# Kernel tuning notes

Measured on AMD Instinct MI355X. Metric: run time of the kernel, lower is better.

The kernel has to match this reference:

```python
import jax, jax.numpy as jnp
import numpy as np

B, C_IN, T_IN = 128, 128, 2500
C_OUT, K, STRIDE, PAD = 64, 27, 4, 13  # T_out = 625
BN_EPS = 1e-5
SURROGATE_ALPHA = 4.0


def binarize_weight(w):
    """1-bit (XNOR-Net style) weight quantization with straight-through estimator.
    w: (O, I, K). Per-output-channel scale = mean |w|."""
    alpha = jnp.mean(jnp.abs(w), axis=(1, 2), keepdims=True)
    wq = jnp.sign(w) * alpha
    return w + jax.lax.stop_gradient(wq - w)


def spike(x):
    """Heaviside spike with sigmoid surrogate gradient (STE)."""
    hard = (x > 0).astype(x.dtype)
    soft = jax.nn.sigmoid(SURROGATE_ALPHA * x)
    return soft + jax.lax.stop_gradient(hard - soft)


def setup_inputs() -> dict:
    key = jax.random.key(0)
    ks = jax.random.split(key, 8)
    scale_conv = 1.0 / np.sqrt(C_IN * K)
    scale_lin = 1.0 / np.sqrt(C_OUT)
    return {
        "x": jax.random.normal(ks[0], (B, C_IN, T_IN), dtype=jnp.float32),
        "conv_w": jax.random.normal(ks[1], (C_OUT, C_IN, K), dtype=jnp.float32) * scale_conv,
        "conv_b": jnp.zeros((C_OUT,), dtype=jnp.float32),
        "bn_gamma": jnp.ones((C_OUT,), dtype=jnp.float32),
        "bn_beta": jnp.zeros((C_OUT,), dtype=jnp.float32),
        "bn_mean": jax.random.normal(ks[2], (C_OUT,), dtype=jnp.float32) * 0.1,
        "bn_var": jax.random.uniform(ks[3], (C_OUT,), dtype=jnp.float32, minval=0.5, maxval=1.5),
        "wq": jax.random.normal(ks[4], (C_OUT, C_OUT), dtype=jnp.float32) * scale_lin,
        "wk": jax.random.normal(ks[5], (C_OUT, C_OUT), dtype=jnp.float32) * scale_lin,
        "wv": jax.random.normal(ks[6], (C_OUT, C_OUT), dtype=jnp.float32) * scale_lin,
        "wo": jax.random.normal(ks[7], (C_OUT, C_OUT), dtype=jnp.float32) * scale_lin,
    }


def reference(x, conv_w, conv_b, bn_gamma, bn_beta, bn_mean, bn_var, wq, wk, wv, wo):
    # --- 1-bit quantized conv1d, stride 4 ---
    w_bin = binarize_weight(conv_w)
    y = jax.lax.conv_general_dilated(
        x, w_bin, window_strides=(STRIDE,), padding=[(PAD, PAD)],
        dimension_numbers=("NCH", "OIH", "NCH"))
    y = y + conv_b[None, :, None]  # (B, C_OUT, 625)

    # --- BatchNorm1d (inference stats) + ELU ---
    inv = jax.lax.rsqrt(bn_var + BN_EPS)
    y = (y - bn_mean[None, :, None]) * (inv * bn_gamma)[None, :, None] + bn_beta[None, :, None]
    y = jax.nn.elu(y)

    # --- Global spiking attention (single head) ---
    s = spike(y)                                   # (B, C, T) binary spikes
    q = jnp.einsum("oc,bct->bot", wq, s)           # (B, C, T)
    k = jnp.einsum("oc,bct->bot", wk, s)
    v = jnp.einsum("oc,bct->bot", wv, y)
    scores = jnp.einsum("bct,bcs->bts", q, k) / jnp.sqrt(jnp.asarray(C_OUT, y.dtype))
    attn = jax.nn.softmax(scores, axis=-1)         # (B, T, T)
    ctx = jnp.einsum("bts,bcs->bct", attn, v)      # (B, C, T)
    out = y + jnp.einsum("oc,bct->bot", wo, ctx)   # residual
    return out
```

## Files before the change

kernel.cpp:

```cpp
#include <hip/hip_runtime.h>
#include <math.h>

#define B_    128
#define CIN   128
#define TIN   2500
#define COUT  64
#define KW    27
#define TOUT  625
#define TPAD  640
#define CTT   32
#define GROWS 152

typedef __bf16 bf16x8 __attribute__((ext_vector_type(8)));
typedef float  f32x4  __attribute__((ext_vector_type(4)));
typedef float  f32x16 __attribute__((ext_vector_type(16)));

__device__ __forceinline__ unsigned short f32_to_bf16_rne(float v) {
    unsigned u = __float_as_uint(v);
    u += 0x7FFFu + ((u >> 16) & 1u);
    return (unsigned short)(u >> 16);
}

__device__ __forceinline__ f32x4 mfma_bf16(bf16x8 a, bf16x8 b, f32x4 c) {
    return __builtin_amdgcn_mfma_f32_16x16x32_bf16(a, b, c, 0, 0, 0);
}

__global__ void prep_kernel(const float* __restrict__ w,
                            const float* __restrict__ wq, const float* __restrict__ wk,
                            const float* __restrict__ wv, const float* __restrict__ wo,
                            const float* __restrict__ conv_b, const float* __restrict__ gamma_,
                            const float* __restrict__ beta_, const float* __restrict__ mean_,
                            const float* __restrict__ var_,
                            unsigned* __restrict__ sgn2,
                            unsigned short* __restrict__ w3_h, unsigned short* __restrict__ w3_l,
                            unsigned short* __restrict__ wo_h, unsigned short* __restrict__ wo_l,
                            float* __restrict__ scA, float* __restrict__ scB) {
    int blk = blockIdx.x, tid = threadIdx.x;
    if (blk < 64) {
        __shared__ float red[256];
        const float* wrow = w + (size_t)blk * (CIN * KW);
        float s = 0.f;
        for (int idx = tid; idx < CIN * KW; idx += 256) s += fabsf(wrow[idx]);
        red[tid] = s;
        __syncthreads();
        for (int st = 128; st > 0; st >>= 1) {
            if (tid < st) red[tid] += red[tid + st];
            __syncthreads();
        }
        if (tid == 0) {
            float alpha = red[0] / (float)(CIN * KW);
            float inv = rsqrtf(var_[blk] + 1e-5f);
            float G = gamma_[blk] * inv;
            scA[blk] = alpha * G;
            scB[blk] = (conv_b[blk] - mean_[blk]) * G + beta_[blk];
        }
        for (int t = tid; t < KW * 4; t += 256) {
            int kk = t >> 2, kg = t & 3;
            unsigned u = 0;
#pragma unroll
            for (int cs = 0; cs < 4; cs++) {
#pragma unroll
                for (int j = 0; j < 8; j++) {
                    int c = cs * 32 + kg * 8 + j;
                    float v = wrow[c * KW + kk];
                    unsigned bit = (v > 0.f) ? 0u : 1u;
                    u |= bit << (cs * 8 + j);
                }
            }
            sgn2[(kk * 4 + kg) * 64 + blk] = u;
        }
    } else if (blk < 67) {
        const float* srcs[3] = {wq, wk, wv};
        const float* src = srcs[blk - 64];
        unsigned short* dh = w3_h + (size_t)(blk - 64) * 4096;
        unsigned short* dl = w3_l + (size_t)(blk - 64) * 4096;
        for (int idx = tid; idx < 4096; idx += 256) {
            float v = src[idx];
            unsigned short h = f32_to_bf16_rne(v);
            float hf = __uint_as_float((unsigned)h << 16);
            dh[idx] = h;
            dl[idx] = f32_to_bf16_rne(v - hf);
        }
    } else {
        for (int idx = tid; idx < 4096; idx += 256) {
            float v = wo[idx];
            unsigned short h = f32_to_bf16_rne(v);
            float hf = __uint_as_float((unsigned)h << 16);
            wo_h[idx] = h;
            wo_l[idx] = f32_to_bf16_rne(v - hf);
        }
    }
}

__global__ __launch_bounds__(256, 4) void conv_kernel(
    const float* __restrict__ x, const unsigned* __restrict__ sgn2,
    const float* __restrict__ scA, const float* __restrict__ scB,
    const unsigned short* __restrict__ w3_h, const unsigned short* __restrict__ w3_l,
    float* __restrict__ y_out,
    unsigned short* __restrict__ q_h, unsigned short* __restrict__ k_h,
    unsigned short* __restrict__ vT_h)
{
    __shared__ __align__(16) unsigned short xhi[GROWS * 128];
    __shared__ __align__(16) unsigned long long sgnlut[16];
    unsigned short* y_sh = xhi;
    unsigned short* s_sh = xhi + 2048;
    unsigned short* q_sh = xhi + 4096;
    unsigned short* k_sh = xhi + 6144;
    unsigned short* v_sh = xhi + 8192;
    float* part_sh = (float*)(xhi + 10240);

    int tid = threadIdx.x;
    int id = blockIdx.x + 20 * blockIdx.y;
    int nid = (id & 7) * 320 + (id >> 3);
    int b = nid / 20;
    int t0 = (nid - b * 20) * CTT;

    if (tid < 16) {
        unsigned long long e = 0;
#pragma unroll
        for (int j = 0; j < 4; ++j) {
            unsigned long long h = ((tid >> j) & 1) ? 0xBF80ull : 0x3F80ull;
            e |= h << (16 * j);
        }
        sgnlut[tid] = e;
    }

    const float* xb = x + (size_t)b * CIN * TIN;
    int gbase = 4 * t0 - 13;
    for (int task = tid; task < 16 * GROWS; task += 256) {
        int c8 = task / GROWS, gl = task - c8 * GROWS;
        int g = gbase + gl;
        bool valid = (gl < 151) && ((unsigned)g < (unsigned)TIN);
        float vs[8];
#pragma unroll
        for (int j = 0; j < 8; j++)
            vs[j] = valid ? xb[(size_t)(c8 * 8 + j) * TIN + g] : 0.f;
        union { unsigned u[4]; uint4 q; } H;
#pragma unroll
        for (int j = 0; j < 4; j++) {
            unsigned short h0 = f32_to_bf16_rne(vs[2 * j]);
            unsigned short h1 = f32_to_bf16_rne(vs[2 * j + 1]);
            H.u[j] = (unsigned)h0 | ((unsigned)h1 << 16);
        }
        int c8p = c8 ^ ((gl >> 2) & 15);
        *(uint4*)(xhi + gl * 128 + c8p * 8) = H.q;
    }
    __syncthreads();

    int wave = tid >> 6, lane = tid & 63;
    int oh = wave & 1, ch = wave >> 1;
    int o0w = oh * 32;
    int lo = lane & 31;
    int kg1 = lane >> 5;

    f32x16 acc = {0.f};
    const unsigned* sgb = sgn2 + o0w + lo;
    unsigned w0 = sgb[kg1 * 64];
    unsigned w1 = sgb[(kg1 + 2) * 64];

#pragma unroll 1
    for (int kk = 0; kk < KW; ++kk) {
        unsigned n0 = 0, n1 = 0;
        if (kk < KW - 1) {
            n0 = sgb[((kk + 1) * 4 + kg1) * 64];
            n1 = sgb[((kk + 1) * 4 + kg1 + 2) * 64];
        }
        int gl = 4 * lo + kk;
        int rot = (gl >> 2) & 15;
        const unsigned short* xr = xhi + gl * 128;
#pragma unroll
        for (int ks = 0; ks < 4; ++ks) {
            int oct = ch * 8 + ks * 2 + kg1;
            int c8p = oct ^ rot;
            bf16x8 bx = *(const bf16x8*)(xr + c8p * 8);
            unsigned wsel = (ks & 1) ? w1 : w0;
            unsigned byte = (wsel >> (8 * (ch * 2 + (ks >> 1)))) & 0xFFu;
            union { unsigned long long u[2]; bf16x8 v; } A;
            A.u[0] = sgnlut[byte & 15u];
            A.u[1] = sgnlut[byte >> 4];
            acc = __builtin_amdgcn_mfma_f32_32x32x16_bf16(A.v, bx, acc, 0, 0, 0);
        }
        w0 = n0; w1 = n1;
    }
    __syncthreads();

    if (ch == 1) {
        float* p = part_sh + oh * 1024 + lane;
#pragma unroll
        for (int r = 0; r < 16; ++r) p[r * 64] = acc[r];
    }
    __syncthreads();

    if (ch == 0) {
        const float* p = part_sh + oh * 1024 + lane;
        int t_g = t0 + lo;
        bool tv = t_g < TOUT;
#pragma unroll
        for (int g2 = 0; g2 < 4; ++g2) {
            unsigned long long yp = 0, sp = 0;
#pragma unroll
            for (int j = 0; j < 4; ++j) {
                int r = g2 * 4 + j;
                float v = acc[r] + p[r * 64];
                int o = o0w + 4 * kg1 + 8 * g2 + j;
                float s = v * scA[o] + scB[o];
                float yv = s > 0.f ? s : expm1f(s);
                if (tv) {
                    y_out[((size_t)b * COUT + o) * TOUT + t_g] = yv;
                    yp |= (unsigned long long)f32_to_bf16_rne(yv) << (16 * j);
                    if (yv > 0.f) sp |= 0x3F80ull << (16 * j);
                }
            }
            int c8 = 4 * oh + g2;
            int idx = lo * 64 + ((c8 ^ (lo & 7)) << 3) + 4 * kg1;
            *(unsigned long long*)(y_sh + idx) = yp;
            *(unsigned long long*)(s_sh + idx) = sp;
        }
    }
    __syncthreads();

    int quad = lane >> 4, col = lane & 15;
    int o0 = wave * 16;
    bf16x8 sf[2][2], yf[2][2];
#pragma unroll
    for (int tt = 0; tt < 2; ++tt)
#pragma unroll
        for (int ks = 0; ks < 2; ++ks) {
            int tl = tt * 16 + col;
            int idx = tl * 64 + (((ks * 4 + quad) ^ (tl & 7)) << 3);
            sf[tt][ks] = *(const bf16x8*)(s_sh + idx);
            yf[tt][ks] = *(const bf16x8*)(y_sh + idx);
        }
    size_t wofs = (size_t)(o0 + col) * 64 + quad * 8;
    f32x4 qa[2], ka[2], va[2];
#pragma unroll
    for (int tt = 0; tt < 2; ++tt) {
        qa[tt] = (f32x4){0.f, 0.f, 0.f, 0.f};
        ka[tt] = (f32x4){0.f, 0.f, 0.f, 0.f};
        va[tt] = (f32x4){0.f, 0.f, 0.f, 0.f};
    }
#pragma unroll
    for (int ks = 0; ks < 2; ++ks) {
        bf16x8 aqh = *(const bf16x8*)(w3_h + wofs + ks * 32);
        bf16x8 aql = *(const bf16x8*)(w3_l + wofs + ks * 32);
        bf16x8 akh = *(const bf16x8*)(w3_h + 4096 + wofs + ks * 32);
        bf16x8 akl = *(const bf16x8*)(w3_l + 4096 + wofs + ks * 32);
        bf16x8 avh = *(const bf16x8*)(w3_h + 8192 + wofs + ks * 32);
        bf16x8 avl = *(const bf16x8*)(w3_l + 8192 + wofs + ks * 32);
#pragma unroll
        for (int tt = 0; tt < 2; ++tt) {
            qa[tt] = mfma_bf16(aqh, sf[tt][ks], qa[tt]);
            qa[tt] = mfma_bf16(aql, sf[tt][ks], qa[tt]);
            ka[tt] = mfma_bf16(akh, sf[tt][ks], ka[tt]);
            ka[tt] = mfma_bf16(akl, sf[tt][ks], ka[tt]);
            va[tt] = mfma_bf16(avh, yf[tt][ks], va[tt]);
            va[tt] = mfma_bf16(avl, yf[tt][ks], va[tt]);
        }
    }
    int c8w = (o0 >> 3) + (quad >> 1);
    int cof = (quad & 1) * 4;
#pragma unroll
    for (int tt = 0; tt < 2; ++tt) {
        int tl = tt * 16 + col;
        int idx = tl * 64 + ((c8w ^ (tl & 7)) << 3) + cof;
        unsigned long long qp = 0, kp = 0;
#pragma unroll
        for (int r = 0; r < 4; ++r) {
            qp |= (unsigned long long)f32_to_bf16_rne(qa[tt][r]) << (16 * r);
            kp |= (unsigned long long)f32_to_bf16_rne(ka[tt][r]) << (16 * r);
        }
        *(unsigned long long*)(q_sh + idx) = qp;
        *(unsigned long long*)(k_sh + idx) = kp;
#pragma unroll
        for (int r = 0; r < 4; ++r) {
            int c = o0 + quad * 4 + r;
            int vidx = c * 32 + (((tt * 2 + (col >> 3)) ^ quad) << 3) + (col & 7);
            v_sh[vidx] = f32_to_bf16_rne(va[tt][r]);
        }
    }
    __syncthreads();

    {
        int tl = tid >> 3, seg = tid & 7;
        int idx = tl * 64 + ((seg ^ (tl & 7)) << 3);
        uint4 qv = *(const uint4*)(q_sh + idx);
        uint4 kv = *(const uint4*)(k_sh + idx);
        size_t go = ((size_t)b * TPAD + t0 + tl) * 64 + seg * 8;
        *(uint4*)(q_h + go) = qv;
        *(uint4*)(k_h + go) = kv;
        int c = tid >> 2, ts = tid & 3;
        int vidx = c * 32 + ((ts ^ ((c >> 2) & 3)) << 3);
        uint4 vv = *(const uint4*)(v_sh + vidx);
        *(uint4*)(vT_h + ((size_t)b * 64 + c) * TPAD + t0 + ts * 8) = vv;
    }
}

__global__ __launch_bounds__(512, 3) void attn_kernel(
    const unsigned short* __restrict__ q_h, const unsigned short* __restrict__ k_h,
    const unsigned short* __restrict__ vT_h, const float* __restrict__ y,
    const unsigned short* __restrict__ wo_h, const unsigned short* __restrict__ wo_l,
    float* __restrict__ out)
{
    __shared__ __align__(16) float sc_sh[16 * 648];
    __shared__ float ctx_sh[2 * 64 * 17];
    __shared__ float rden[16];

    int tid = threadIdx.x;
    int id = blockIdx.x + 40 * blockIdx.y;
    int nid = (id & 7) * 640 + (id >> 3);
    int b = nid / 40;
    int t0 = (nid - b * 40) * 16;

    int wave = tid >> 6, lane = tid & 63;
    int quad = lane >> 4, nlo = lane & 15;

    const unsigned short* qb = q_h + ((size_t)b * TPAD + t0 + nlo) * 64 + quad * 8;
    bf16x8 qa0 = *(const bf16x8*)(qb);
    bf16x8 qa1 = *(const bf16x8*)(qb + 32);
    const unsigned short* kbase = k_h + (size_t)b * TPAD * 64 + quad * 8;
#pragma unroll 5
    for (int nt = 0; nt < 5; ++nt) {
        int s = wave * 80 + nt * 16 + nlo;
        const unsigned short* krow = kbase + (size_t)s * 64;
        bf16x8 kb0 = *(const bf16x8*)(krow);
        bf16x8 kb1 = *(const bf16x8*)(krow + 32);
        f32x4 acc = {0.f, 0.f, 0.f, 0.f};
        acc = mfma_bf16(qa0, kb0, acc);
        acc = mfma_bf16(qa1, kb1, acc);
#pragma unroll
        for (int r = 0; r < 4; ++r)
            sc_sh[(quad * 4 + r) * 648 + s] = acc[r] * 0.125f;
    }
    __syncthreads();

    int ti1 = tid >> 5, sg = tid & 31;
    float* srow = &sc_sh[ti1 * 648];
    float mx = -3.0e38f;
    for (int s = sg; s < TOUT; s += 32) mx = fmaxf(mx, srow[s]);
#pragma unroll
    for (int off = 16; off >= 1; off >>= 1) mx = fmaxf(mx, __shfl_xor(mx, off));

    unsigned short* prow = (unsigned short*)srow;
    float sum = 0.f;
#pragma unroll
    for (int k2 = 0; k2 < 10; ++k2) {
        int s = 2 * sg + 64 * k2;
        float2 v2 = *(const float2*)(srow + s);
        float e0 = (s     < TOUT) ? __expf(v2.x - mx) : 0.f;
        float e1 = (s + 1 < TOUT) ? __expf(v2.y - mx) : 0.f;
        sum += e0 + e1;
        unsigned u0 = __float_as_uint(e0); u0 += 0x7FFFu + ((u0 >> 16) & 1u);
        unsigned u1 = __float_as_uint(e1); u1 += 0x7FFFu + ((u1 >> 16) & 1u);
        *(unsigned*)(prow + s) = (u0 >> 16) | (u1 & 0xFFFF0000u);
    }
#pragma unroll
    for (int off = 16; off >= 1; off >>= 1) sum += __shfl_xor(sum, off);
    if (sg == 0) rden[ti1] = 1.f / sum;
    __syncthreads();

    int cw = (wave & 3) * 16, kh = wave >> 2;
    const unsigned short* vb = vT_h + ((size_t)b * 64 + cw + nlo) * TPAD;
    const unsigned short* pb = (const unsigned short*)sc_sh + nlo * 1296;
    f32x4 cacc = {0.f, 0.f, 0.f, 0.f};
    int ks0 = kh * 10;
#pragma unroll 5
    for (int i = 0; i < 10; ++i) {
        int ks = ks0 + i;
        bf16x8 pv = *(const bf16x8*)(pb + ks * 32 + quad * 8);
        bf16x8 v8 = *(const bf16x8*)(vb + ks * 32 + quad * 8);
        cacc = mfma_bf16(pv, v8, cacc);
    }
#pragma unroll
    for (int r = 0; r < 4; ++r)
        ctx_sh[kh * 1088 + (cw + nlo) * 17 + quad * 4 + r] = cacc[r] * rden[quad * 4 + r];
    __syncthreads();

    if (wave < 4) {
        const unsigned short* woh = wo_h + (size_t)(wave * 16 + nlo) * 64 + quad * 8;
        const unsigned short* wol = wo_l + (size_t)(wave * 16 + nlo) * 64 + quad * 8;
        f32x4 oacc = {0.f, 0.f, 0.f, 0.f};
#pragma unroll
        for (int ks = 0; ks < 2; ++ks) {
            union { unsigned short u[8]; bf16x8 v; } Bc;
#pragma unroll
            for (int j = 0; j < 8; ++j) {
                int c = ks * 32 + quad * 8 + j;
                float cv = ctx_sh[c * 17 + nlo] + ctx_sh[1088 + c * 17 + nlo];
                Bc.u[j] = f32_to_bf16_rne(cv);
            }
            bf16x8 ah = *(const bf16x8*)(woh + ks * 32);
            bf16x8 al = *(const bf16x8*)(wol + ks * 32);
            oacc = mfma_bf16(ah, Bc.v, oacc);
            oacc = mfma_bf16(al, Bc.v, oacc);
        }
        int t_g = t0 + nlo;
        if (t_g < TOUT) {
#pragma unroll
            for (int r = 0; r < 4; ++r) {
                int o = wave * 16 + quad * 4 + r;
                size_t off = ((size_t)b * COUT + o) * TOUT + t_g;
                out[off] = y[off] + oacc[r];
            }
        }
    }
}

extern "C" void kernel_launch(void* const* d_in, const int* in_sizes, int n_in,
                              void* d_out, int out_size, void* d_ws, size_t ws_size,
                              hipStream_t stream) {
    const float* x        = (const float*)d_in[0];
    const float* conv_w   = (const float*)d_in[1];
    const float* conv_b   = (const float*)d_in[2];
    const float* bn_gamma = (const float*)d_in[3];
    const float* bn_beta  = (const float*)d_in[4];
    const float* bn_mean  = (const float*)d_in[5];
    const float* bn_var   = (const float*)d_in[6];
    const float* wq       = (const float*)d_in[7];
    const float* wk       = (const float*)d_in[8];
    const float* wv       = (const float*)d_in[9];
    const float* wo       = (const float*)d_in[10];
    float* out = (float*)d_out;
    float* ws  = (float*)d_ws;

    unsigned* sgn2        = (unsigned*)ws;
    float* scA            = ws + 110656;
    float* scB            = ws + 110720;
    unsigned short* w3_h  = (unsigned short*)(ws + 110848);
    unsigned short* w3_l  = (unsigned short*)(ws + 116992);
    unsigned short* wo_h  = (unsigned short*)(ws + 123136);
    unsigned short* wo_l  = (unsigned short*)(ws + 125184);
    float* yb             = ws + 131072;
    unsigned short* q_h   = (unsigned short*)(ws + 5251072);
    unsigned short* k_h   = (unsigned short*)(ws + 7872512);
    unsigned short* vT_h  = (unsigned short*)(ws + 10493952);

    hipLaunchKernelGGL(prep_kernel, dim3(68), dim3(256), 0, stream,
                       conv_w, wq, wk, wv, wo, conv_b, bn_gamma, bn_beta, bn_mean, bn_var,
                       sgn2, w3_h, w3_l, wo_h, wo_l, scA, scB);
    hipLaunchKernelGGL(conv_kernel, dim3(20, 128), dim3(256), 0, stream,
                       x, sgn2, scA, scB, w3_h, w3_l, yb, q_h, k_h, vT_h);
    hipLaunchKernelGGL(attn_kernel, dim3(40, 128), dim3(512), 0, stream,
                       q_h, k_h, vT_h, yb, wo_h, wo_l, out);
}
```

Baseline: 427.0 us.

## Compute softmax in registers from MFMA accumulators with bf16 LDS probabilities

Scaling, row max, exponentials and row sums are now done directly on the QK^T MFMA accumulators in registers. Per-wave partial maxima and sums are combined through small LDS arrays instead of a full fp32 score buffer. Only bf16 probabilities are written to LDS, roughly halving the score buffer and dropping one full pass over it. The launch-bounds occupancy hint rises from 3 to 8 blocks, which forces a tighter register budget and risks spills.

```diff
diff --git a/kernel.cpp b/kernel.cpp
--- a/kernel.cpp
+++ b/kernel.cpp
@@ -295,15 +295,16 @@
     }
 }
 
-__global__ __launch_bounds__(512, 3) void attn_kernel(
+__global__ __launch_bounds__(512, 8) void attn_kernel(
     const unsigned short* __restrict__ q_h, const unsigned short* __restrict__ k_h,
     const unsigned short* __restrict__ vT_h, const float* __restrict__ y,
     const unsigned short* __restrict__ wo_h, const unsigned short* __restrict__ wo_l,
     float* __restrict__ out)
 {
-    __shared__ __align__(16) float sc_sh[16 * 648];
+    __shared__ __align__(16) unsigned short P_lds[16 * 648];
+    __shared__ __align__(16) float pmax_sh[16 * 8];
+    __shared__ __align__(16) float psum_sh[16 * 8];
     __shared__ float ctx_sh[2 * 64 * 17];
-    __shared__ float rden[16];
 
     int tid = threadIdx.x;
     int id = blockIdx.x + 40 * blockIdx.y;
@@ -318,49 +319,91 @@
     bf16x8 qa0 = *(const bf16x8*)(qb);
     bf16x8 qa1 = *(const bf16x8*)(qb + 32);
     const unsigned short* kbase = k_h + (size_t)b * TPAD * 64 + quad * 8;
+    f32x4 acc[5];
 #pragma unroll 5
     for (int nt = 0; nt < 5; ++nt) {
         int s = wave * 80 + nt * 16 + nlo;
         const unsigned short* krow = kbase + (size_t)s * 64;
         bf16x8 kb0 = *(const bf16x8*)(krow);
         bf16x8 kb1 = *(const bf16x8*)(krow + 32);
-        f32x4 acc = {0.f, 0.f, 0.f, 0.f};
-        acc = mfma_bf16(qa0, kb0, acc);
-        acc = mfma_bf16(qa1, kb1, acc);
+        f32x4 a = {0.f, 0.f, 0.f, 0.f};
+        a = mfma_bf16(qa0, kb0, a);
+        a = mfma_bf16(qa1, kb1, a);
+        acc[nt] = a;
+    }
+
+    float rmx[4] = {-3.0e38f, -3.0e38f, -3.0e38f, -3.0e38f};
+#pragma unroll
+    for (int nt = 0; nt < 5; ++nt) {
+        int s = wave * 80 + nt * 16 + nlo;
+        bool v = s < TOUT;
+#pragma unroll
+        for (int r = 0; r < 4; ++r) {
+            float sc = acc[nt][r] * 0.125f;
+            acc[nt][r] = sc;
+            if (v) rmx[r] = fmaxf(rmx[r], sc);
+        }
+    }
+#pragma unroll
+    for (int off = 1; off < 16; off <<= 1)
+#pragma unroll
+        for (int r = 0; r < 4; ++r) rmx[r] = fmaxf(rmx[r], __shfl_xor(rmx[r], off));
+    if (nlo == 0) {
+#pragma unroll
+        for (int r = 0; r < 4; ++r) pmax_sh[(quad * 4 + r) * 8 + wave] = rmx[r];
+    }
+    __syncthreads();
+
+    float rsum[4] = {0.f, 0.f, 0.f, 0.f};
+    float rowm[4];
+#pragma unroll
+    for (int r = 0; r < 4; ++r) {
+        const float4* pm = (const float4*)&pmax_sh[(quad * 4 + r) * 8];
+        float4 a = pm[0], c = pm[1];
+        rowm[r] = fmaxf(fmaxf(fmaxf(a.x, a.y), fmaxf(a.z, a.w)),
+                        fmaxf(fmaxf(c.x, c.y), fmaxf(c.z, c.w)));
+    }
+#pragma unroll
+    for (int nt = 0; nt < 5; ++nt) {
+        int s = wave * 80 + nt * 16 + nlo;
+        bool v = s < TOUT;
+#pragma unroll
+        for (int r = 0; r < 4; ++r) {
+            float e = v ? __expf(acc[nt][r] - rowm[r]) : 0.f;
+            acc[nt][r] = e;
+            rsum[r] += e;
+        }
+    }
+#pragma unroll
+    for (int off = 1; off < 16; off <<= 1)
+#pragma unroll
+        for (int r = 0; r < 4; ++r) rsum[r] += __shfl_xor(rsum[r], off);
+    if (nlo == 0) {
+#pragma unroll
+        for (int r = 0; r < 4; ++r) psum_sh[(quad * 4 + r) * 8 + wave] = rsum[r];
+    }
+
+    unsigned short* pw = P_lds;
+#pragma unroll
+    for (int nt = 0; nt < 5; ++nt) {
+        int s = wave * 80 + nt * 16 + nlo;
 #pragma unroll
         for (int r = 0; r < 4; ++r)
-            sc_sh[(quad * 4 + r) * 648 + s] = acc[r] * 0.125f;
-    }
-    __syncthreads();
-
-    int ti1 = tid >> 5, sg = tid & 31;
-    float* srow = &sc_sh[ti1 * 648];
-    float mx = -3.0e38f;
-    for (int s = sg; s < TOUT; s += 32) mx = fmaxf(mx, srow[s]);
-#pragma unroll
-    for (int off = 16; off >= 1; off >>= 1) mx = fmaxf(mx, __shfl_xor(mx, off));
-
-    unsigned short* prow = (unsigned short*)srow;
-    float sum = 0.f;
-#pragma unroll
-    for (int k2 = 0; k2 < 10; ++k2) {
-        int s = 2 * sg + 64 * k2;
-        float2 v2 = *(const float2*)(srow + s);
-        float e0 = (s     < TOUT) ? __expf(v2.x - mx) : 0.f;
-        float e1 = (s + 1 < TOUT) ? __expf(v2.y - mx) : 0.f;
-        sum += e0 + e1;
-        unsigned u0 = __float_as_uint(e0); u0 += 0x7FFFu + ((u0 >> 16) & 1u);
-        unsigned u1 = __float_as_uint(e1); u1 += 0x7FFFu + ((u1 >> 16) & 1u);
-        *(unsigned*)(prow + s) = (u0 >> 16) | (u1 & 0xFFFF0000u);
-    }
-#pragma unroll
-    for (int off = 16; off >= 1; off >>= 1) sum += __shfl_xor(sum, off);
-    if (sg == 0) rden[ti1] = 1.f / sum;
-    __syncthreads();
+            pw[(quad * 4 + r) * 648 + s] = f32_to_bf16_rne(acc[nt][r]);
+    }
+    __syncthreads();
+
+    float rden_r[4];
+#pragma unroll
+    for (int r = 0; r < 4; ++r) {
+        const float4* ps = (const float4*)&psum_sh[(quad * 4 + r) * 8];
+        float4 a = ps[0], c = ps[1];
+        rden_r[r] = 1.f / (((a.x + a.y) + (a.z + a.w)) + ((c.x + c.y) + (c.z + c.w)));
+    }
 
     int cw = (wave & 3) * 16, kh = wave >> 2;
     const unsigned short* vb = vT_h + ((size_t)b * 64 + cw + nlo) * TPAD;
-    const unsigned short* pb = (const unsigned short*)sc_sh + nlo * 1296;
+    const unsigned short* pb = P_lds + nlo * 648;
     f32x4 cacc = {0.f, 0.f, 0.f, 0.f};
     int ks0 = kh * 10;
 #pragma unroll 5
@@ -372,7 +415,7 @@
     }
 #pragma unroll
     for (int r = 0; r < 4; ++r)
-        ctx_sh[kh * 1088 + (cw + nlo) * 17 + quad * 4 + r] = cacc[r] * rden[quad * 4 + r];
+        ctx_sh[kh * 1088 + (cw + nlo) * 17 + quad * 4 + r] = cacc[r] * rden_r[r];
     __syncthreads();
 
     if (wave < 4) {
```

Result: no change. 425.8 us (-0.3%).
